# Kernel optimization log

Measured on AMD Instinct MI355X. Metric: run time of the kernel, lower is better.

## Reference

```python
import jax, jax.numpy as jnp
import numpy as np
import math

DIM = 1024
NUM_HEADS = 16
HEAD_DIM = DIM // NUM_HEADS  # 64
LAYER_IDX = 12
LAMBDA_INIT = 0.8 - 0.6 * math.exp(-0.3 * (LAYER_IDX - 1))
LN_EPS = 1e-5


def setup_inputs() -> dict:
    key = jax.random.key(0)
    ks = jax.random.split(key, 11)
    B, S = 2, 2048
    x = jax.random.normal(ks[0], (B, S, DIM), dtype=jnp.float32)
    s = 1.0 / math.sqrt(DIM)
    Wq = jax.random.normal(ks[1], (DIM, 2 * DIM), dtype=jnp.float32) * s
    Wk = jax.random.normal(ks[2], (DIM, 2 * DIM), dtype=jnp.float32) * s
    Wv = jax.random.normal(ks[3], (DIM, DIM), dtype=jnp.float32) * s
    Wo = jax.random.normal(ks[4], (DIM, DIM), dtype=jnp.float32) * s
    lambda_q1 = jax.random.normal(ks[5], (HEAD_DIM,), dtype=jnp.float32) * 0.1
    lambda_k1 = jax.random.normal(ks[6], (HEAD_DIM,), dtype=jnp.float32) * 0.1
    lambda_q2 = jax.random.normal(ks[7], (HEAD_DIM,), dtype=jnp.float32) * 0.1
    lambda_k2 = jax.random.normal(ks[8], (HEAD_DIM,), dtype=jnp.float32) * 0.1
    gamma = jnp.ones((DIM,), dtype=jnp.float32)
    beta = jnp.zeros((DIM,), dtype=jnp.float32)
    return {"x": x, "Wq": Wq, "Wk": Wk, "Wv": Wv, "Wo": Wo,
            "lambda_q1": lambda_q1, "lambda_k1": lambda_k1,
            "lambda_q2": lambda_q2, "lambda_k2": lambda_k2,
            "gamma": gamma, "beta": beta}


def reference(x, Wq, Wk, Wv, Wo, lambda_q1, lambda_k1, lambda_q2, lambda_k2, gamma, beta):
    B, S, _ = x.shape
    scaling = HEAD_DIM ** (-0.5)
    # projections: [B,S,H,2d] / [B,S,H,d] -> [B,H,S,*]
    Q = (x @ Wq).reshape(B, S, NUM_HEADS, 2 * HEAD_DIM).transpose(0, 2, 1, 3)
    K = (x @ Wk).reshape(B, S, NUM_HEADS, 2 * HEAD_DIM).transpose(0, 2, 1, 3)
    V = (x @ Wv).reshape(B, S, NUM_HEADS, HEAD_DIM).transpose(0, 2, 1, 3)
    # lambda scalar
    lamb = (jnp.exp(jnp.sum(lambda_q1 * lambda_k1))
            - jnp.exp(jnp.sum(lambda_q2 * lambda_k2)) + LAMBDA_INIT)
    Q1, Q2 = jnp.split(Q, 2, axis=-1)
    K1, K2 = jnp.split(K, 2, axis=-1)
    A1 = jnp.einsum('bhqd,bhkd->bhqk', Q1, K1) * scaling
    A2 = jnp.einsum('bhqd,bhkd->bhqk', Q2, K2) * scaling
    attn = jax.nn.softmax(A1, axis=-1) - lamb * jax.nn.softmax(A2, axis=-1)
    out = jnp.einsum('bhqk,bhkd->bhqd', attn, V)  # [B,H,S,d]
    out = out.transpose(0, 2, 1, 3).reshape(B, S, DIM)
    out = out @ Wo
    # LayerNorm
    mu = jnp.mean(out, axis=-1, keepdims=True)
    var = jnp.var(out, axis=-1, keepdims=True)
    out = (out - mu) * jax.lax.rsqrt(var + LN_EPS) * gamma + beta
    return out
```

## Files before the change

### kernel.cpp

```cpp
#include <hip/hip_runtime.h>
#include <hip/hip_bf16.h>

typedef short bf16x8 __attribute__((ext_vector_type(8)));
typedef float f32x4 __attribute__((ext_vector_type(4)));
typedef unsigned short us4v __attribute__((ext_vector_type(4)));
typedef unsigned int uint2v __attribute__((ext_vector_type(2)));

#define DEV static __device__ __forceinline__

DEV float bf2f(unsigned short u){ unsigned int x = ((unsigned int)u)<<16; float f; __builtin_memcpy(&f,&x,4); return f; }
DEV unsigned short f2bf(float f){ unsigned int x; __builtin_memcpy(&x,&f,4); x = (x + 0x7fffu + ((x>>16)&1u)) >> 16; return (unsigned short)x; }

DEV unsigned int pack_trunc(float lo, float hi){
  unsigned int a, b;
  __builtin_memcpy(&a, &lo, 4);
  __builtin_memcpy(&b, &hi, 4);
  return (b & 0xffff0000u) | (a >> 16);
}

DEV void stor(unsigned short* p, float v){ *p = f2bf(v); }
DEV void stor(float* p, float v){ *p = v; }

#if __has_builtin(__builtin_amdgcn_exp2f)
DEV float fexp2(float x){ return __builtin_amdgcn_exp2f(x); }
#else
DEV float fexp2(float x){ return exp2f(x); }
#endif

#if __has_builtin(__builtin_amdgcn_permlane32_swap)
DEV uint2v pl32(unsigned int a, unsigned int b){ return __builtin_amdgcn_permlane32_swap(a, b, false, false); }
#else
DEV uint2v pl32(unsigned int a, unsigned int b){
  unsigned int sa = (unsigned int)__shfl_xor((int)a, 32);
  unsigned int sb = (unsigned int)__shfl_xor((int)b, 32);
  bool hi = (threadIdx.x & 32) != 0;
  uint2v r; r[0] = hi ? sb : a; r[1] = hi ? b : sa; return r;
}
#endif
#if __has_builtin(__builtin_amdgcn_permlane16_swap)
DEV uint2v pl16(unsigned int a, unsigned int b){ return __builtin_amdgcn_permlane16_swap(a, b, false, false); }
#else
DEV uint2v pl16(unsigned int a, unsigned int b){
  unsigned int sa = (unsigned int)__shfl_xor((int)a, 16);
  unsigned int sb = (unsigned int)__shfl_xor((int)b, 16);
  bool hi = (threadIdx.x & 16) != 0;
  uint2v r; r[0] = hi ? sb : a; r[1] = hi ? b : sa; return r;
}
#endif

#define GLOAD_LDS16(gptr, lptr) \
  __builtin_amdgcn_global_load_lds((__attribute__((address_space(1))) void*)(gptr), \
      (__attribute__((address_space(3))) void*)(lptr), 16, 0, 0)

template<typename OutT>
__global__ __launch_bounds__(256) void gemm_bt(
    const unsigned short* __restrict__ A,
    const unsigned short* __restrict__ Bt,
    OutT* __restrict__ C, int M, int N, int K)
{
  __shared__ unsigned short As[128*32];
  __shared__ unsigned short Bs[128*32];
  const int tid = threadIdx.x;
  const int w = tid>>6, l = tid&63, g = l>>4, q = l&15;
  const int m0 = blockIdx.x*128, n0 = blockIdx.y*128;
  f32x4 acc[4][4];
  const f32x4 fz = {0.f,0.f,0.f,0.f};
  for (int i=0;i<4;i++) for(int j=0;j<4;j++) acc[i][j] = fz;
  for (int k0 = 0; k0 < K; k0 += 32) {
    __syncthreads();
    #pragma unroll
    for (int r = 0; r < 2; ++r) {
      int p = r*4096 + tid*16;
      int row = p>>6, colb = p&63;
      const char* ga = (const char*)(A  + (size_t)(m0+row)*K + k0) + colb;
      const char* gb = (const char*)(Bt + (size_t)(n0+row)*K + k0) + colb;
      GLOAD_LDS16(ga, (char*)As + r*4096 + w*1024);
      GLOAD_LDS16(gb, (char*)Bs + r*4096 + w*1024);
    }
    __syncthreads();
    bf16x8 af[4], bfr[4];
    #pragma unroll
    for (int i=0;i<4;i++){
      af[i]  = *(const bf16x8*)&As[((w>>1)*64 + i*16 + q)*32 + g*8];
      bfr[i] = *(const bf16x8*)&Bs[((w&1)*64 + i*16 + q)*32 + g*8];
    }
    #pragma unroll
    for (int i=0;i<4;i++)
      #pragma unroll
      for (int j=0;j<4;j++)
        acc[i][j] = __builtin_amdgcn_mfma_f32_16x16x32_bf16(af[i], bfr[j], acc[i][j], 0,0,0);
  }
  #pragma unroll
  for (int i=0;i<4;i++)
    #pragma unroll
    for (int j=0;j<4;j++)
      #pragma unroll
      for (int v=0;v<4;v++){
        int row = m0 + (w>>1)*64 + i*16 + g*4 + v;
        int col = n0 + (w&1)*64 + j*16 + q;
        stor(&C[(size_t)row*N + col], acc[i][j][v]);
      }
}

__global__ __launch_bounds__(256,4) void diff_attn(
    const unsigned short* __restrict__ Qp,
    const unsigned short* __restrict__ Kp,
    const unsigned short* __restrict__ Vt,
    unsigned short* __restrict__ ao1,
    unsigned short* __restrict__ ao2)
{
  const int LDQ = 5120;
  __shared__ unsigned short Ks0[64*64];
  __shared__ unsigned short Ks1[64*64];
  __shared__ unsigned short Vs0[64*64];
  __shared__ unsigned short Vs1[64*64];
  const int tid = threadIdx.x, w = tid>>6, l = tid&63, g = l>>4, q = l&15;
  const int qb = blockIdx.x, h = blockIdx.y;
  const int s = blockIdx.z >> 1, b = blockIdx.z & 1;
  const int b2048 = b*2048;
  const int qrow0 = b2048 + qb*128 + w*32;
  const f32x4 fz = {0.f,0.f,0.f,0.f};
  const short one_bf = (short)0x3f80;
  const bf16x8 ones = {one_bf,one_bf,one_bf,one_bf,one_bf,one_bf,one_bf,one_bf};
  unsigned short* aout = s ? ao2 : ao1;

  bf16x8 qf[2][2];
  #pragma unroll
  for (int qh=0; qh<2; ++qh){
    const unsigned short* qp = Qp + (size_t)(qrow0 + qh*16 + q)*LDQ + h*128 + s*64;
    #pragma unroll
    for (int kf=0;kf<2;kf++)
      qf[qh][kf] = *(const bf16x8*)(qp + kf*32 + g*8);
  }
  f32x4 acc[2][4];
  f32x4 acc_s[2];
  #pragma unroll
  for (int qh=0;qh<2;qh++){
    acc_s[qh]=fz;
    #pragma unroll
    for (int i=0;i<4;i++) acc[qh][i]=fz;
  }

  auto STAGE = [&](unsigned short* Kd, unsigned short* Vd, int kt){
    #pragma unroll
    for (int ii=0; ii<2; ++ii){
      int krow = w*16 + ii*8 + (l>>3);
      int gr = (l&7) ^ (krow&7);
      const unsigned short* src = Kp + (size_t)(b2048 + kt + krow)*LDQ + h*128 + s*64 + gr*8;
      GLOAD_LDS16(src, (char*)Kd + (w*16 + ii*8)*128);
    }
    #pragma unroll
    for (int jj=0; jj<2; ++jj){
      int vrow = w*16 + jj*8 + (l>>3);
      int gr = (l&7) ^ (vrow&7);
      const unsigned short* src = Vt + (size_t)(h*64 + vrow)*4096 + b2048 + kt + gr*8;
      GLOAD_LDS16(src, (char*)Vd + (w*16 + jj*8)*128);
    }
  };

  auto COMPUTE = [&](const unsigned short* Kr, const unsigned short* Vr){
    const int sw = q & 7;
    unsigned int cc[2][4][2];
    #pragma unroll
    for (int fn=0; fn<4; ++fn) {
      const unsigned short* kr = Kr + (fn*16 + q)*64;
      bf16x8 kb0 = *(const bf16x8*)&kr[((0+g)^sw)*8];
      bf16x8 kb1 = *(const bf16x8*)&kr[((4+g)^sw)*8];
      f32x4 z[2];
      __builtin_amdgcn_s_setprio(1);
      #pragma unroll
      for (int qh=0; qh<2; ++qh){
        f32x4 a = fz;
        a = __builtin_amdgcn_mfma_f32_16x16x32_bf16(kb0, qf[qh][0], a, 0,0,0);
        a = __builtin_amdgcn_mfma_f32_16x16x32_bf16(kb1, qf[qh][1], a, 0,0,0);
        z[qh] = a;
      }
      __builtin_amdgcn_s_setprio(0);
      #pragma unroll
      for (int qh=0; qh<2; ++qh){
        cc[qh][fn][0] = pack_trunc(fexp2(z[qh][0]), fexp2(z[qh][1]));
        cc[qh][fn][1] = pack_trunc(fexp2(z[qh][2]), fexp2(z[qh][3]));
      }
    }

    bf16x8 pa[2][2];
    #pragma unroll
    for (int qh=0; qh<2; ++qh)
      #pragma unroll
      for (int kh=0; kh<2; ++kh){
        unsigned int* u = (unsigned int*)&pa[qh][kh];
        #pragma unroll
        for (int j=0;j<2;j++){
          uint2v d = pl32(cc[qh][2*kh][j], cc[qh][2*kh+1][j]);
          uint2v e = pl16(d[0], d[1]);
          u[j] = e[0]; u[2+j] = e[1];
        }
      }

    __builtin_amdgcn_s_setprio(1);
    #pragma unroll
    for (int kh=0; kh<2; ++kh){
      #pragma unroll
      for (int qh=0; qh<2; ++qh)
        acc_s[qh] = __builtin_amdgcn_mfma_f32_16x16x32_bf16(pa[qh][kh], ones, acc_s[qh], 0,0,0);
      #pragma unroll
      for (int fd=0; fd<4; ++fd){
        bf16x8 vb = *(const bf16x8*)&Vr[(fd*16+q)*64 + ((kh*4+g)^sw)*8];
        #pragma unroll
        for (int qh=0; qh<2; ++qh)
          acc[qh][fd] = __builtin_amdgcn_mfma_f32_16x16x32_bf16(pa[qh][kh], vb, acc[qh][fd], 0,0,0);
      }
    }
    __builtin_amdgcn_s_setprio(0);
  };

  STAGE(Ks0, Vs0, 0);
  __syncthreads();

  for (int t=0; t<32; t+=2) {
    STAGE(Ks1, Vs1, (t+1)*64);
    COMPUTE(Ks0, Vs0);
    __syncthreads();
    if (t+2 < 32) STAGE(Ks0, Vs0, (t+2)*64);
    COMPUTE(Ks1, Vs1);
    if (t+2 < 32) __syncthreads();
  }

  #pragma unroll
  for (int qh=0; qh<2; ++qh){
    float inv[4];
    #pragma unroll
    for (int i=0;i<4;i++) inv[i] = 1.0f/acc_s[qh][i];
    #pragma unroll
    for (int fd=0; fd<4; ++fd)
      #pragma unroll
      for (int i=0;i<4;i++){
        int row = qrow0 + qh*16 + g*4 + i;
        int col = h*64 + fd*16 + q;
        aout[(size_t)row*1024 + col] = f2bf(acc[qh][fd][i]*inv[i]);
      }
  }
}

__global__ __launch_bounds__(256) void combine_k(
    const unsigned short* __restrict__ a1, const unsigned short* __restrict__ a2,
    const float* __restrict__ lambp, unsigned short* __restrict__ out, int n)
{
  int i = (blockIdx.x*256 + threadIdx.x)*8;
  if (i >= n) return;
  float lamb = lambp[0];
  bf16x8 v1 = *(const bf16x8*)(a1+i), v2 = *(const bf16x8*)(a2+i);
  bf16x8 o;
  #pragma unroll
  for (int e=0;e<8;e++)
    o[e] = (short)f2bf(bf2f((unsigned short)v1[e]) - lamb*bf2f((unsigned short)v2[e]));
  *(bf16x8*)(out+i) = o;
}

__global__ __launch_bounds__(256) void f32_to_bf16_k(const float* __restrict__ in, unsigned short* __restrict__ out, int n){
  int i = (blockIdx.x*256 + threadIdx.x)*4;
  if (i >= n) return;
  float4 vv = *(const float4*)(in + i);
  us4v o; o[0]=f2bf(vv.x); o[1]=f2bf(vv.y); o[2]=f2bf(vv.z); o[3]=f2bf(vv.w);
  *(us4v*)(out + i) = o;
}

__global__ void transpose_f32_bf16(const float* __restrict__ in, unsigned short* __restrict__ out, int R, int C, float scale){
  __shared__ unsigned short t[32][33];
  int c0 = blockIdx.x*32, r0 = blockIdx.y*32;
  int x = threadIdx.x, y = threadIdx.y;
  #pragma unroll
  for (int d=0; d<32; d+=8) t[y+d][x] = f2bf(in[(size_t)(r0+y+d)*C + c0 + x] * scale);
  __syncthreads();
  #pragma unroll
  for (int d=0; d<32; d+=8) out[(size_t)(c0+y+d)*R + r0 + x] = t[x][y+d];
}

__global__ void transpose_bf16_ld(const unsigned short* __restrict__ in, unsigned short* __restrict__ out, int R, int C, int ldin){
  __shared__ unsigned short t[32][33];
  int c0 = blockIdx.x*32, r0 = blockIdx.y*32;
  int x = threadIdx.x, y = threadIdx.y;
  #pragma unroll
  for (int d=0; d<32; d+=8) t[y+d][x] = in[(size_t)(r0+y+d)*ldin + c0 + x];
  __syncthreads();
  #pragma unroll
  for (int d=0; d<32; d+=8) out[(size_t)(c0+y+d)*R + r0 + x] = t[x][y+d];
}

__global__ void lamb_k(const float* lq1, const float* lk1, const float* lq2, const float* lk2, float* out){
  int i = threadIdx.x;
  float a = lq1[i]*lk1[i], c = lq2[i]*lk2[i];
  #pragma unroll
  for (int o=32;o>0;o>>=1){ a += __shfl_down(a,o); c += __shfl_down(c,o); }
  if (i==0) out[0] = expf(a) - expf(c) + 0.7778700995592560f;
}

__global__ __launch_bounds__(256) void ln_k(const float* __restrict__ in, const float* __restrict__ gam,
                                            const float* __restrict__ bet, float* __restrict__ out){
  int row = blockIdx.x, t = threadIdx.x;
  const float4* rp = (const float4*)(in + (size_t)row*1024);
  float4 v4 = rp[t];
  float s = v4.x+v4.y+v4.z+v4.w;
  float ss = v4.x*v4.x+v4.y*v4.y+v4.z*v4.z+v4.w*v4.w;
  #pragma unroll
  for (int o=1;o<64;o<<=1){ s += __shfl_xor(s,o); ss += __shfl_xor(ss,o); }
  __shared__ float red[8];
  int w = t>>6, l = t&63;
  if (l==0){ red[w]=s; red[4+w]=ss; }
  __syncthreads();
  s = red[0]+red[1]+red[2]+red[3];
  ss = red[4]+red[5]+red[6]+red[7];
  float mean = s*(1.0f/1024.0f);
  float var = ss*(1.0f/1024.0f) - mean*mean;
  float rstd = rsqrtf(var + 1e-5f);
  float4 gv = ((const float4*)gam)[t], bv = ((const float4*)bet)[t];
  float4 o;
  o.x = (v4.x-mean)*rstd*gv.x + bv.x;
  o.y = (v4.y-mean)*rstd*gv.y + bv.y;
  o.z = (v4.z-mean)*rstd*gv.z + bv.z;
  o.w = (v4.w-mean)*rstd*gv.w + bv.w;
  ((float4*)(out + (size_t)row*1024))[t] = o;
}

extern "C" void kernel_launch(void* const* d_in, const int* in_sizes, int n_in,
                              void* d_out, int out_size, void* d_ws, size_t ws_size,
                              hipStream_t stream) {
  const float* x     = (const float*)d_in[0];
  const float* Wq    = (const float*)d_in[1];
  const float* Wk    = (const float*)d_in[2];
  const float* Wv    = (const float*)d_in[3];
  const float* Wo    = (const float*)d_in[4];
  const float* lq1   = (const float*)d_in[5];
  const float* lk1   = (const float*)d_in[6];
  const float* lq2   = (const float*)d_in[7];
  const float* lk2   = (const float*)d_in[8];
  const float* gamma = (const float*)d_in[9];
  const float* beta  = (const float*)d_in[10];
  float* out = (float*)d_out;

  char* ws = (char*)d_ws;
  unsigned short* xb    = (unsigned short*)(ws);
  unsigned short* WcatT = (unsigned short*)(ws + 8388608);
  unsigned short* WoT   = (unsigned short*)(ws + 18874368);
  unsigned short* QKV   = (unsigned short*)(ws + 20971520);
  unsigned short* Vtb   = (unsigned short*)(ws + 62914560);
  unsigned short* AO1   = (unsigned short*)(ws + 71303168);
  unsigned short* AO2   = (unsigned short*)(ws + 79691776);
  unsigned short* AOc   = (unsigned short*)(ws + 88080384);
  float*          proj  = (float*)(ws + 20971520);
  float*          lambp = (float*)(ws + 96468992);

  const float QSCALE = 0.125f * 1.4426950408889634f;
  dim3 tb(32,8);
  f32_to_bf16_k<<<4096, 256, 0, stream>>>(x, xb, 4194304);
  transpose_f32_bf16<<<dim3(64,32), tb, 0, stream>>>(Wq, WcatT,             1024, 2048, QSCALE);
  transpose_f32_bf16<<<dim3(64,32), tb, 0, stream>>>(Wk, WcatT + 2048*1024, 1024, 2048, 1.0f);
  transpose_f32_bf16<<<dim3(32,32), tb, 0, stream>>>(Wv, WcatT + 4096*1024, 1024, 1024, 1.0f);
  transpose_f32_bf16<<<dim3(32,32), tb, 0, stream>>>(Wo, WoT, 1024, 1024, 1.0f);
  lamb_k<<<1, 64, 0, stream>>>(lq1, lk1, lq2, lk2, lambp);

  gemm_bt<unsigned short><<<dim3(32,40), 256, 0, stream>>>(xb, WcatT, QKV, 4096, 5120, 1024);
  transpose_bf16_ld<<<dim3(32,128), tb, 0, stream>>>(QKV + 4096, Vtb, 4096, 1024, 5120);

  diff_attn<<<dim3(16,16,4), 256, 0, stream>>>(QKV, QKV + 2048, Vtb, AO1, AO2);
  combine_k<<<2048, 256, 0, stream>>>(AO1, AO2, lambp, AOc, 4194304);

  gemm_bt<float><<<dim3(32,8), 256, 0, stream>>>(AOc, WoT, proj, 4096, 1024, 1024);
  ln_k<<<4096, 256, 0, stream>>>(proj, gamma, beta, out);
}
```

Baseline: 207.0 us.

## Use smaller-tile output GEMM, merge weight transposes, use perm for bf16 pack

```diff
diff --git a/kernel.cpp b/kernel.cpp
--- a/kernel.cpp
+++ b/kernel.cpp
@@ -11,12 +11,21 @@
 DEV float bf2f(unsigned short u){ unsigned int x = ((unsigned int)u)<<16; float f; __builtin_memcpy(&f,&x,4); return f; }
 DEV unsigned short f2bf(float f){ unsigned int x; __builtin_memcpy(&x,&f,4); x = (x + 0x7fffu + ((x>>16)&1u)) >> 16; return (unsigned short)x; }
 
+#if __has_builtin(__builtin_amdgcn_perm)
+DEV unsigned int pack_trunc(float lo, float hi){
+  unsigned int a, b;
+  __builtin_memcpy(&a, &lo, 4);
+  __builtin_memcpy(&b, &hi, 4);
+  return __builtin_amdgcn_perm(b, a, 0x07060302u);
+}
+#else
 DEV unsigned int pack_trunc(float lo, float hi){
   unsigned int a, b;
   __builtin_memcpy(&a, &lo, 4);
   __builtin_memcpy(&b, &hi, 4);
   return (b & 0xffff0000u) | (a >> 16);
 }
+#endif
 
 DEV void stor(unsigned short* p, float v){ *p = f2bf(v); }
 DEV void stor(float* p, float v){ *p = v; }
@@ -99,6 +108,57 @@
         int row = m0 + (w>>1)*64 + i*16 + g*4 + v;
         int col = n0 + (w&1)*64 + j*16 + q;
         stor(&C[(size_t)row*N + col], acc[i][j][v]);
+      }
+}
+
+__global__ __launch_bounds__(256) void gemm_bt_64(
+    const unsigned short* __restrict__ A,
+    const unsigned short* __restrict__ Bt,
+    float* __restrict__ C, int M, int N, int K)
+{
+  __shared__ unsigned short As[64*32];
+  __shared__ unsigned short Bs[128*32];
+  const int tid = threadIdx.x;
+  const int w = tid>>6, l = tid&63, g = l>>4, q = l&15;
+  const int m0 = blockIdx.x*64, n0 = blockIdx.y*128;
+  f32x4 acc[4][2];
+  const f32x4 fz = {0.f,0.f,0.f,0.f};
+  for (int i=0;i<4;i++) for(int j=0;j<2;j++) acc[i][j] = fz;
+  for (int k0 = 0; k0 < K; k0 += 32) {
+    __syncthreads();
+    {
+      int row = tid>>2, colb = (tid&3)*16;
+      const char* ga = (const char*)(A + (size_t)(m0+row)*K + k0) + colb;
+      GLOAD_LDS16(ga, (char*)As + tid*16);
+    }
+    #pragma unroll
+    for (int r = 0; r < 2; ++r) {
+      int p = r*4096 + tid*16;
+      int row = p>>6, colb = p&63;
+      const char* gb = (const char*)(Bt + (size_t)(n0+row)*K + k0) + colb;
+      GLOAD_LDS16(gb, (char*)Bs + r*4096 + w*1024);
+    }
+    __syncthreads();
+    bf16x8 af[4], bfr[2];
+    #pragma unroll
+    for (int i=0;i<4;i++) af[i] = *(const bf16x8*)&As[(i*16 + q)*32 + g*8];
+    #pragma unroll
+    for (int j=0;j<2;j++) bfr[j] = *(const bf16x8*)&Bs[(w*32 + j*16 + q)*32 + g*8];
+    #pragma unroll
+    for (int i=0;i<4;i++)
+      #pragma unroll
+      for (int j=0;j<2;j++)
+        acc[i][j] = __builtin_amdgcn_mfma_f32_16x16x32_bf16(af[i], bfr[j], acc[i][j], 0,0,0);
+  }
+  #pragma unroll
+  for (int i=0;i<4;i++)
+    #pragma unroll
+    for (int j=0;j<2;j++)
+      #pragma unroll
+      for (int v=0;v<4;v++){
+        int row = m0 + i*16 + g*4 + v;
+        int col = n0 + w*32 + j*16 + q;
+        C[(size_t)row*N + col] = acc[i][j][v];
       }
 }
 
@@ -265,15 +325,26 @@
   *(us4v*)(out + i) = o;
 }
 
-__global__ void transpose_f32_bf16(const float* __restrict__ in, unsigned short* __restrict__ out, int R, int C, float scale){
+__global__ void transpose_weights(const float* __restrict__ Wq, const float* __restrict__ Wk,
+                                  const float* __restrict__ Wv, const float* __restrict__ Wo,
+                                  unsigned short* __restrict__ WcatT, unsigned short* __restrict__ WoT,
+                                  float qscale){
   __shared__ unsigned short t[32][33];
-  int c0 = blockIdx.x*32, r0 = blockIdx.y*32;
+  int bid = blockIdx.x;
+  const float* in; unsigned short* out; int C; float scale = 1.0f;
+  if (bid < 2048){ in = Wq; out = WcatT;             C = 2048; scale = qscale; }
+  else if (bid < 4096){ in = Wk; out = WcatT + 2048*1024; C = 2048; bid -= 2048; }
+  else if (bid < 5120){ in = Wv; out = WcatT + 4096*1024; C = 1024; bid -= 4096; }
+  else { in = Wo; out = WoT; C = 1024; bid -= 5120; }
+  int xt = (C == 2048) ? (bid & 63) : (bid & 31);
+  int yt = (C == 2048) ? (bid >> 6) : (bid >> 5);
+  int c0 = xt*32, r0 = yt*32;
   int x = threadIdx.x, y = threadIdx.y;
   #pragma unroll
   for (int d=0; d<32; d+=8) t[y+d][x] = f2bf(in[(size_t)(r0+y+d)*C + c0 + x] * scale);
   __syncthreads();
   #pragma unroll
-  for (int d=0; d<32; d+=8) out[(size_t)(c0+y+d)*R + r0 + x] = t[x][y+d];
+  for (int d=0; d<32; d+=8) out[(size_t)(c0+y+d)*1024 + r0 + x] = t[x][y+d];
 }
 
 __global__ void transpose_bf16_ld(const unsigned short* __restrict__ in, unsigned short* __restrict__ out, int R, int C, int ldin){
@@ -353,10 +424,7 @@
   const float QSCALE = 0.125f * 1.4426950408889634f;
   dim3 tb(32,8);
   f32_to_bf16_k<<<4096, 256, 0, stream>>>(x, xb, 4194304);
-  transpose_f32_bf16<<<dim3(64,32), tb, 0, stream>>>(Wq, WcatT,             1024, 2048, QSCALE);
-  transpose_f32_bf16<<<dim3(64,32), tb, 0, stream>>>(Wk, WcatT + 2048*1024, 1024, 2048, 1.0f);
-  transpose_f32_bf16<<<dim3(32,32), tb, 0, stream>>>(Wv, WcatT + 4096*1024, 1024, 1024, 1.0f);
-  transpose_f32_bf16<<<dim3(32,32), tb, 0, stream>>>(Wo, WoT, 1024, 1024, 1.0f);
+  transpose_weights<<<6144, tb, 0, stream>>>(Wq, Wk, Wv, Wo, WcatT, WoT, QSCALE);
   lamb_k<<<1, 64, 0, stream>>>(lq1, lk1, lq2, lk2, lambp);
 
   gemm_bt<unsigned short><<<dim3(32,40), 256, 0, stream>>>(xb, WcatT, QKV, 4096, 5120, 1024);
@@ -365,6 +433,6 @@
   diff_attn<<<dim3(16,16,4), 256, 0, stream>>>(QKV, QKV + 2048, Vtb, AO1, AO2);
   combine_k<<<2048, 256, 0, stream>>>(AO1, AO2, lambp, AOc, 4194304);
 
-  gemm_bt<float><<<dim3(32,8), 256, 0, stream>>>(AOc, WoT, proj, 4096, 1024, 1024);
+  gemm_bt_64<<<dim3(64,8), 256, 0, stream>>>(AOc, WoT, proj, 4096, 1024, 1024);
   ln_k<<<4096, 256, 0, stream>>>(proj, gamma, beta, out);
 }
```

After: 197.6 us. -4.5%, faster.
